# Performance work log

Hardware: AMD Instinct MI355X
Metric: run time of the kernel (lower is better)

The kernel has to match this reference:

```python
import jax, jax.numpy as jnp
import numpy as np

N = 50000
NFEAT = 512
HID = 128
E = 1_600_000


def spmm(row, col, val, dense):
    # sparse [N,N] (COO) @ dense [N,D] -> [N,D]
    gathered = val[:, None] * dense[col]           # [E, D]
    return jax.ops.segment_sum(gathered, row, num_segments=N)


def setup_inputs() -> dict:
    key = jax.random.key(0)
    ks = jax.random.split(key, 12)
    x = jax.random.normal(ks[0], (N, NFEAT), dtype=jnp.float32)
    adj_row = jax.random.randint(ks[1], (E,), 0, N, dtype=jnp.int32)
    adj_col = jax.random.randint(ks[2], (E,), 0, N, dtype=jnp.int32)
    adj_val = jax.random.uniform(ks[3], (E,), dtype=jnp.float32)
    adj_inv_row = jax.random.randint(ks[4], (E,), 0, N, dtype=jnp.int32)
    adj_inv_col = jax.random.randint(ks[5], (E,), 0, N, dtype=jnp.int32)
    adj_inv_val = jax.random.uniform(ks[6], (E,), dtype=jnp.float32)
    # Glorot-ish init for GCN weights
    W1 = jax.random.normal(ks[7], (NFEAT, HID), dtype=jnp.float32) * (1.0 / np.sqrt(NFEAT))
    b1 = jnp.zeros((HID,), dtype=jnp.float32)
    W2 = jax.random.normal(ks[8], (HID, NFEAT), dtype=jnp.float32) * (1.0 / np.sqrt(HID))
    b2 = jnp.zeros((NFEAT,), dtype=jnp.float32)
    return dict(x=x, adj_row=adj_row, adj_col=adj_col, adj_val=adj_val,
                adj_inv_row=adj_inv_row, adj_inv_col=adj_inv_col, adj_inv_val=adj_inv_val,
                W1=W1, b1=b1, W2=W2, b2=b2)


def reference(x, adj_row, adj_col, adj_val, adj_inv_row, adj_inv_col, adj_inv_val,
              W1, b1, W2, b2):
    # Encoder GCN layer: relu( adj @ (x @ W1) + b1 )
    h = jax.nn.relu(spmm(adj_row, adj_col, adj_val, x @ W1) + b1)   # [N, 128]
    embedding = h
    # Decoder GCN layer: relu( adj_inv @ (h @ W2) + b2 )
    out = jax.nn.relu(spmm(adj_inv_row, adj_inv_col, adj_inv_val, h @ W2) + b2)  # [N, nfeat]
    return (out, embedding)
```

## Files before the change

### kernel.cpp

```cpp
#include <hip/hip_runtime.h>

#define NN     50000
#define NFEAT  512
#define HIDD   128
#define NE     1600000
#define NB     ((NN + 255) / 256)
#define NPART  8
#define RPP    (NN / NPART)

typedef __attribute__((ext_vector_type(8))) short    bf16x8;
typedef __attribute__((ext_vector_type(4))) float    f32x4;
typedef __attribute__((ext_vector_type(4))) unsigned short us4;

__device__ inline unsigned short f2bf(float f) {
  unsigned int u = __float_as_uint(f);
  u += 0x7FFFu + ((u >> 16) & 1u);
  return (unsigned short)(u >> 16);
}

__device__ inline float bf2f(unsigned short h) {
  return __uint_as_float((unsigned int)h << 16);
}

__device__ inline void fma4(float4& a, float v, const float4& d) {
  a.x = fmaf(v, d.x, a.x);
  a.y = fmaf(v, d.y, a.y);
  a.z = fmaf(v, d.z, a.z);
  a.w = fmaf(v, d.w, a.w);
}

__device__ inline void fma4b(float4& a, float v, us4 d) {
  a.x = fmaf(v, bf2f(d[0]), a.x);
  a.y = fmaf(v, bf2f(d[1]), a.y);
  a.z = fmaf(v, bf2f(d[2]), a.z);
  a.w = fmaf(v, bf2f(d[3]), a.w);
}

__global__ __launch_bounds__(256) void hist_kernel(
    const int* __restrict__ row, int* __restrict__ counts, int e) {
  int i = blockIdx.x * blockDim.x + threadIdx.x;
  if (i < e) atomicAdd(&counts[row[i]], 1);
}

__global__ __launch_bounds__(256) void block_sum_kernel(
    const int* __restrict__ counts, int* __restrict__ bsum, int n) {
  __shared__ int ws[4];
  int i = blockIdx.x * 256 + threadIdx.x;
  int lane = threadIdx.x & 63, wid = threadIdx.x >> 6;
  int v = (i < n) ? counts[i] : 0;
#pragma unroll
  for (int off = 32; off > 0; off >>= 1) v += __shfl_down(v, off, 64);
  if (lane == 0) ws[wid] = v;
  __syncthreads();
  if (threadIdx.x == 0) bsum[blockIdx.x] = ws[0] + ws[1] + ws[2] + ws[3];
}

__global__ __launch_bounds__(256) void scan_partials_kernel(
    int* __restrict__ bsum, int* __restrict__ rowptr, int nb, int nfull) {
  __shared__ int ws[4];
  int t = threadIdx.x;
  int lane = t & 63, wid = t >> 6;
  int v = (t < nb) ? bsum[t] : 0;
  int incl = v;
#pragma unroll
  for (int off = 1; off < 64; off <<= 1) {
    int u = __shfl_up(incl, off, 64);
    if (lane >= off) incl += u;
  }
  if (lane == 63) ws[wid] = incl;
  __syncthreads();
  int wprefix = 0;
  for (int w = 0; w < wid; ++w) wprefix += ws[w];
  incl += wprefix;
  if (t < nb) bsum[t] = incl - v;
  if (t == nb - 1) rowptr[nfull] = incl;
}

__global__ __launch_bounds__(256) void scan_apply_kernel(
    int* __restrict__ counts, const int* __restrict__ bsum,
    int* __restrict__ rowptr, int n) {
  __shared__ int ws[4];
  int i = blockIdx.x * 256 + threadIdx.x;
  int lane = threadIdx.x & 63, wid = threadIdx.x >> 6;
  int v = (i < n) ? counts[i] : 0;
  int incl = v;
#pragma unroll
  for (int off = 1; off < 64; off <<= 1) {
    int u = __shfl_up(incl, off, 64);
    if (lane >= off) incl += u;
  }
  if (lane == 63) ws[wid] = incl;
  __syncthreads();
  int wprefix = 0;
  for (int w = 0; w < wid; ++w) wprefix += ws[w];
  int excl = bsum[blockIdx.x] + wprefix + (incl - v);
  if (i < n) { rowptr[i] = excl; counts[i] = excl; }
}

__global__ __launch_bounds__(256) void scatter_part_kernel(
    const int* __restrict__ row, const int* __restrict__ col,
    const float* __restrict__ val, int* __restrict__ wptr,
    int2* __restrict__ pairs, int e) {
  int part = blockIdx.x & (NPART - 1);
  int q    = blockIdx.x >> 3;
  int Q    = gridDim.x >> 3;
  int lo = part * RPP, hi = lo + RPP;
  for (int i = q * 256 + threadIdx.x; i < e; i += Q * 256) {
    int r = row[i];
    if (r >= lo && r < hi) {
      int p = atomicAdd(&wptr[r], 1);
      pairs[p] = make_int2(col[i], __float_as_int(val[i]));
    }
  }
}

template <bool DB16, bool EPI, bool WF32, bool WB16>
__global__ __launch_bounds__(256) void spmm_kernel(
    const int* __restrict__ rowptr, const int2* __restrict__ pairs,
    const void* __restrict__ dense, const float* __restrict__ bias,
    float* __restrict__ outf, unsigned short* __restrict__ outb, int n) {
  int r = blockIdx.x * 8 + (threadIdx.x >> 5);
  if (r >= n) return;
  int c4 = (threadIdx.x & 31);
  int s = rowptr[r], e = rowptr[r + 1];
  float4 a0 = make_float4(0.f, 0.f, 0.f, 0.f);
  float4 a1 = a0, a2 = a0, a3 = a0;
  int j = s;
  if constexpr (DB16) {
    const unsigned short* d16 = (const unsigned short*)dense;
    for (; j + 8 <= e; j += 8) {
      int2 p0 = pairs[j + 0], p1 = pairs[j + 1], p2 = pairs[j + 2], p3 = pairs[j + 3];
      int2 p4 = pairs[j + 4], p5 = pairs[j + 5], p6 = pairs[j + 6], p7 = pairs[j + 7];
      us4 d0 = *(const us4*)(d16 + (size_t)p0.x * 128 + c4 * 4);
      us4 d1 = *(const us4*)(d16 + (size_t)p1.x * 128 + c4 * 4);
      us4 d2 = *(const us4*)(d16 + (size_t)p2.x * 128 + c4 * 4);
      us4 d3 = *(const us4*)(d16 + (size_t)p3.x * 128 + c4 * 4);
      us4 d4 = *(const us4*)(d16 + (size_t)p4.x * 128 + c4 * 4);
      us4 d5 = *(const us4*)(d16 + (size_t)p5.x * 128 + c4 * 4);
      us4 d6 = *(const us4*)(d16 + (size_t)p6.x * 128 + c4 * 4);
      us4 d7 = *(const us4*)(d16 + (size_t)p7.x * 128 + c4 * 4);
      fma4b(a0, __int_as_float(p0.y), d0);
      fma4b(a1, __int_as_float(p1.y), d1);
      fma4b(a2, __int_as_float(p2.y), d2);
      fma4b(a3, __int_as_float(p3.y), d3);
      fma4b(a0, __int_as_float(p4.y), d4);
      fma4b(a1, __int_as_float(p5.y), d5);
      fma4b(a2, __int_as_float(p6.y), d6);
      fma4b(a3, __int_as_float(p7.y), d7);
    }
    for (; j < e; ++j) {
      int2 ev = pairs[j];
      us4 d = *(const us4*)(d16 + (size_t)ev.x * 128 + c4 * 4);
      fma4b(a0, __int_as_float(ev.y), d);
    }
  } else {
    const float4* dense4 = (const float4*)dense;
    for (; j + 8 <= e; j += 8) {
      int2 p0 = pairs[j + 0], p1 = pairs[j + 1], p2 = pairs[j + 2], p3 = pairs[j + 3];
      int2 p4 = pairs[j + 4], p5 = pairs[j + 5], p6 = pairs[j + 6], p7 = pairs[j + 7];
      float4 d0 = dense4[(size_t)p0.x * 32 + c4];
      float4 d1 = dense4[(size_t)p1.x * 32 + c4];
      float4 d2 = dense4[(size_t)p2.x * 32 + c4];
      float4 d3 = dense4[(size_t)p3.x * 32 + c4];
      float4 d4 = dense4[(size_t)p4.x * 32 + c4];
      float4 d5 = dense4[(size_t)p5.x * 32 + c4];
      float4 d6 = dense4[(size_t)p6.x * 32 + c4];
      float4 d7 = dense4[(size_t)p7.x * 32 + c4];
      fma4(a0, __int_as_float(p0.y), d0);
      fma4(a1, __int_as_float(p1.y), d1);
      fma4(a2, __int_as_float(p2.y), d2);
      fma4(a3, __int_as_float(p3.y), d3);
      fma4(a0, __int_as_float(p4.y), d4);
      fma4(a1, __int_as_float(p5.y), d5);
      fma4(a2, __int_as_float(p6.y), d6);
      fma4(a3, __int_as_float(p7.y), d7);
    }
    for (; j < e; ++j) {
      int2 ev = pairs[j];
      float4 d = dense4[(size_t)ev.x * 32 + c4];
      fma4(a0, __int_as_float(ev.y), d);
    }
  }
  float4 acc;
  acc.x = (a0.x + a1.x) + (a2.x + a3.x);
  acc.y = (a0.y + a1.y) + (a2.y + a3.y);
  acc.z = (a0.z + a1.z) + (a2.z + a3.z);
  acc.w = (a0.w + a1.w) + (a2.w + a3.w);
  if (EPI) {
    float4 b = ((const float4*)bias)[c4];
    acc.x = fmaxf(acc.x + b.x, 0.f);
    acc.y = fmaxf(acc.y + b.y, 0.f);
    acc.z = fmaxf(acc.z + b.z, 0.f);
    acc.w = fmaxf(acc.w + b.w, 0.f);
  }
  if (WF32)
    *(float4*)(outf + (size_t)r * 128 + c4 * 4) = acc;
  if (WB16) {
    us4 h = {f2bf(acc.x), f2bf(acc.y), f2bf(acc.z), f2bf(acc.w)};
    *(us4*)(outb + (size_t)r * 128 + c4 * 4) = h;
  }
}

template <int K, int N, bool EPI, bool ABF16, bool OUTB>
__global__ __launch_bounds__(256) void gemm_mfma_kernel(
    const void* __restrict__ Av, const float* __restrict__ B,
    const float* __restrict__ bias, void* __restrict__ Cv, int M) {
  __shared__ __align__(16) unsigned short Alds[4096];
  __shared__ __align__(16) unsigned short Blds[4096];
  int tid = threadIdx.x;
  int lane = tid & 63, wid = tid >> 6;
  int wm = wid >> 1, wn = wid & 1;
  int rowBase = blockIdx.x * 128;
  int colBase = blockIdx.y * 128;
  int kg = tid & 7, mrow = tid >> 3;
  int aquad = kg >> 1, aj0 = (kg & 1) * 4;
  int bn = tid & 127, kh = tid >> 7;
  int NTb = bn >> 4, nloc = bn & 15;

  f32x4 acc[4][4];
#pragma unroll
  for (int mt = 0; mt < 4; ++mt)
#pragma unroll
    for (int nt = 0; nt < 4; ++nt)
      acc[mt][nt] = (f32x4){0.f, 0.f, 0.f, 0.f};

  for (int kb = 0; kb < K; kb += 32) {
    float4 av[4];
    us4 av16[4];
    if constexpr (ABF16) {
      const unsigned short* A = (const unsigned short*)Av;
#pragma unroll
      for (int p = 0; p < 4; ++p) {
        int r = rowBase + p * 32 + mrow;
        av16[p] = (r < M) ? *(const us4*)(A + (size_t)r * K + kb + kg * 4)
                          : (us4){0, 0, 0, 0};
      }
    } else {
      const float* A = (const float*)Av;
#pragma unroll
      for (int p = 0; p < 4; ++p) {
        int r = rowBase + p * 32 + mrow;
        av[p] = (r < M) ? *(const float4*)(A + (size_t)r * K + kb + kg * 4)
                        : make_float4(0.f, 0.f, 0.f, 0.f);
      }
    }
    float bv[4][4];
#pragma unroll
    for (int p = 0; p < 4; ++p) {
      int k = p * 8 + kh * 4;
#pragma unroll
      for (int i = 0; i < 4; ++i)
        bv[p][i] = B[(size_t)(kb + k + i) * N + colBase + bn];
    }
    __syncthreads();
#pragma unroll
    for (int p = 0; p < 4; ++p) {
      int m = p * 32 + mrow;
      int MT = m >> 4, mloc = m & 15;
      us4 h;
      if constexpr (ABF16) h = av16[p];
      else h = (us4){f2bf(av[p].x), f2bf(av[p].y), f2bf(av[p].z), f2bf(av[p].w)};
      *(us4*)&Alds[(((MT * 4 + aquad) * 16 + mloc) << 3) + aj0] = h;
    }
#pragma unroll
    for (int p = 0; p < 4; ++p) {
      us4 h = {f2bf(bv[p][0]), f2bf(bv[p][1]), f2bf(bv[p][2]), f2bf(bv[p][3])};
      *(us4*)&Blds[(((NTb * 4 + p) * 16 + nloc) << 3) + kh * 4] = h;
    }
    __syncthreads();
    bf16x8 af[4], bf[4];
#pragma unroll
    for (int mt = 0; mt < 4; ++mt)
      af[mt] = *(bf16x8*)&Alds[(((wm * 4 + mt) * 64 + lane)) << 3];
#pragma unroll
    for (int nt = 0; nt < 4; ++nt)
      bf[nt] = *(bf16x8*)&Blds[(((wn * 4 + nt) * 64 + lane)) << 3];
#pragma unroll
    for (int mt = 0; mt < 4; ++mt)
#pragma unroll
      for (int nt = 0; nt < 4; ++nt)
        acc[mt][nt] = __builtin_amdgcn_mfma_f32_16x16x32_bf16(
            af[mt], bf[nt], acc[mt][nt], 0, 0, 0);
  }
  int cquad = lane >> 4, cn = lane & 15;
#pragma unroll
  for (int nt = 0; nt < 4; ++nt) {
    int col = colBase + wn * 64 + nt * 16 + cn;
    float bb = EPI ? bias[col] : 0.f;
#pragma unroll
    for (int mt = 0; mt < 4; ++mt) {
      int r0 = rowBase + wm * 64 + mt * 16 + cquad * 4;
#pragma unroll
      for (int i = 0; i < 4; ++i) {
        int r = r0 + i;
        if (r < M) {
          float o = acc[mt][nt][i];
          if (EPI) o = fmaxf(o + bb, 0.f);
          if constexpr (OUTB)
            ((unsigned short*)Cv)[(size_t)r * N + col] = f2bf(o);
          else
            ((float*)Cv)[(size_t)r * N + col] = o;
        }
      }
    }
  }
}

extern "C" void kernel_launch(void* const* d_in, const int* in_sizes, int n_in,
                              void* d_out, int out_size, void* d_ws, size_t ws_size,
                              hipStream_t stream) {
  const float* x        = (const float*)d_in[0];
  const int*   adj_row  = (const int*)d_in[1];
  const int*   adj_col  = (const int*)d_in[2];
  const float* adj_val  = (const float*)d_in[3];
  const int*   ainv_row = (const int*)d_in[4];
  const int*   ainv_col = (const int*)d_in[5];
  const float* ainv_val = (const float*)d_in[6];
  const float* W1       = (const float*)d_in[7];
  const float* b1       = (const float*)d_in[8];
  const float* W2       = (const float*)d_in[9];
  const float* b2       = (const float*)d_in[10];

  float* out = (float*)d_out;
  float* emb = out + (size_t)NN * NFEAT;

  size_t off = 0;
  auto carve = [&](size_t bytes) {
    void* p = (char*)d_ws + off;
    off += (bytes + 255) & ~(size_t)255;
    return p;
  };
  unsigned short* Tb   = (unsigned short*)carve((size_t)NN * HIDD * 2);
  unsigned short* H0b  = (unsigned short*)carve((size_t)NN * HIDD * 2);
  int*  rowptr_a = (int*)carve(50004 * 4);
  int*  rowptr_b = (int*)carve(50004 * 4);
  int*  wptr_a   = (int*)carve(50004 * 4);
  int*  wptr_b   = (int*)carve(50004 * 4);
  int*  bsum_a   = (int*)carve(256 * 4);
  int*  bsum_b   = (int*)carve(256 * 4);
  int2* pairs_a  = (int2*)carve((size_t)NE * 8);
  int2* pairs_b  = (int2*)carve((size_t)NE * 8);
  unsigned short* embb = (unsigned short*)((char*)d_ws + off);
  bool full = ws_size >= off + (size_t)NN * HIDD * 2;

  hipMemsetAsync(wptr_a, 0, NN * sizeof(int), stream);
  hipMemsetAsync(wptr_b, 0, NN * sizeof(int), stream);
  hist_kernel<<<NE / 256, 256, 0, stream>>>(adj_row, wptr_a, NE);
  hist_kernel<<<NE / 256, 256, 0, stream>>>(ainv_row, wptr_b, NE);
  block_sum_kernel<<<NB, 256, 0, stream>>>(wptr_a, bsum_a, NN);
  block_sum_kernel<<<NB, 256, 0, stream>>>(wptr_b, bsum_b, NN);
  scan_partials_kernel<<<1, 256, 0, stream>>>(bsum_a, rowptr_a, NB, NN);
  scan_partials_kernel<<<1, 256, 0, stream>>>(bsum_b, rowptr_b, NB, NN);
  scan_apply_kernel<<<NB, 256, 0, stream>>>(wptr_a, bsum_a, rowptr_a, NN);
  scan_apply_kernel<<<NB, 256, 0, stream>>>(wptr_b, bsum_b, rowptr_b, NN);
  scatter_part_kernel<<<2048, 256, 0, stream>>>(adj_row, adj_col, adj_val,
                                                wptr_a, pairs_a, NE);
  scatter_part_kernel<<<2048, 256, 0, stream>>>(ainv_row, ainv_col, ainv_val,
                                                wptr_b, pairs_b, NE);

  gemm_mfma_kernel<NFEAT, HIDD, false, false, true>
      <<<dim3((NN + 127) / 128, 1), 256, 0, stream>>>(x, W1, nullptr, H0b, NN);

  if (full)
    spmm_kernel<true, true, true, true><<<(NN + 7) / 8, 256, 0, stream>>>(
        rowptr_a, pairs_a, H0b, b1, emb, embb, NN);
  else
    spmm_kernel<true, true, true, false><<<(NN + 7) / 8, 256, 0, stream>>>(
        rowptr_a, pairs_a, H0b, b1, emb, nullptr, NN);

  if (full)
    spmm_kernel<true, false, false, true><<<(NN + 7) / 8, 256, 0, stream>>>(
        rowptr_b, pairs_b, embb, nullptr, nullptr, Tb, NN);
  else
    spmm_kernel<false, false, false, true><<<(NN + 7) / 8, 256, 0, stream>>>(
        rowptr_b, pairs_b, emb, nullptr, nullptr, Tb, NN);

  gemm_mfma_kernel<HIDD, NFEAT, true, true, false>
      <<<dim3((NN + 127) / 128, 4), 256, 0, stream>>>(Tb, W2, b2, out, NN);
}
```

Baseline: 711.3 us.

## Record per-edge rank in histogram pass and merge paired CSR-build launches

The histogram kernel now stores each edge's atomicAdd return value as its rank within its row. The scatter pass then places each edge at rowptr[row]+rank without a second round of atomics and without the eight-way row-partitioned multi-pass scan. The two adjacency builds are also merged into single launches using blockIdx.y, which halves the number of launches for each CSR-build stage. In exchange it adds two rank arrays of NE ints (extra workspace and memory traffic), and each pair is written with a 64-bit atomicExch instead of a plain store.

Measured after the change: 684.6 us. 3.8% less time.

```diff
diff --git a/kernel.cpp b/kernel.cpp
--- a/kernel.cpp
+++ b/kernel.cpp
@@ -5,8 +5,6 @@
 #define HIDD   128
 #define NE     1600000
 #define NB     ((NN + 255) / 256)
-#define NPART  8
-#define RPP    (NN / NPART)
 
 typedef __attribute__((ext_vector_type(8))) short    bf16x8;
 typedef __attribute__((ext_vector_type(4))) float    f32x4;
@@ -36,14 +34,22 @@
   a.w = fmaf(v, bf2f(d[3]), a.w);
 }
 
-__global__ __launch_bounds__(256) void hist_kernel(
-    const int* __restrict__ row, int* __restrict__ counts, int e) {
-  int i = blockIdx.x * blockDim.x + threadIdx.x;
-  if (i < e) atomicAdd(&counts[row[i]], 1);
+__global__ __launch_bounds__(256) void hist_rank_kernel(
+    const int* __restrict__ rowA, const int* __restrict__ rowB,
+    int* __restrict__ cntA, int* __restrict__ cntB,
+    int* __restrict__ rnkA, int* __restrict__ rnkB, int e) {
+  const int* row = blockIdx.y ? rowB : rowA;
+  int*       cnt = blockIdx.y ? cntB : cntA;
+  int*       rnk = blockIdx.y ? rnkB : rnkA;
+  int i = blockIdx.x * 256 + threadIdx.x;
+  if (i < e) rnk[i] = atomicAdd(&cnt[row[i]], 1);
 }
 
 __global__ __launch_bounds__(256) void block_sum_kernel(
-    const int* __restrict__ counts, int* __restrict__ bsum, int n) {
+    const int* __restrict__ cntA, const int* __restrict__ cntB,
+    int* __restrict__ bsumA, int* __restrict__ bsumB, int n) {
+  const int* counts = blockIdx.y ? cntB : cntA;
+  int*       bsum   = blockIdx.y ? bsumB : bsumA;
   __shared__ int ws[4];
   int i = blockIdx.x * 256 + threadIdx.x;
   int lane = threadIdx.x & 63, wid = threadIdx.x >> 6;
@@ -56,7 +62,10 @@
 }
 
 __global__ __launch_bounds__(256) void scan_partials_kernel(
-    int* __restrict__ bsum, int* __restrict__ rowptr, int nb, int nfull) {
+    int* __restrict__ bsumA, int* __restrict__ bsumB,
+    int* __restrict__ rpA, int* __restrict__ rpB, int nb, int nfull) {
+  int* bsum   = blockIdx.x ? bsumB : bsumA;
+  int* rowptr = blockIdx.x ? rpB : rpA;
   __shared__ int ws[4];
   int t = threadIdx.x;
   int lane = t & 63, wid = t >> 6;
@@ -77,8 +86,12 @@
 }
 
 __global__ __launch_bounds__(256) void scan_apply_kernel(
-    int* __restrict__ counts, const int* __restrict__ bsum,
-    int* __restrict__ rowptr, int n) {
+    const int* __restrict__ cntA, const int* __restrict__ cntB,
+    const int* __restrict__ bsumA, const int* __restrict__ bsumB,
+    int* __restrict__ rpA, int* __restrict__ rpB, int n) {
+  const int* counts = blockIdx.y ? cntB : cntA;
+  const int* bsum   = blockIdx.y ? bsumB : bsumA;
+  int*       rowptr = blockIdx.y ? rpB : rpA;
   __shared__ int ws[4];
   int i = blockIdx.x * 256 + threadIdx.x;
   int lane = threadIdx.x & 63, wid = threadIdx.x >> 6;
@@ -93,24 +106,29 @@
   __syncthreads();
   int wprefix = 0;
   for (int w = 0; w < wid; ++w) wprefix += ws[w];
-  int excl = bsum[blockIdx.x] + wprefix + (incl - v);
-  if (i < n) { rowptr[i] = excl; counts[i] = excl; }
-}
-
-__global__ __launch_bounds__(256) void scatter_part_kernel(
-    const int* __restrict__ row, const int* __restrict__ col,
-    const float* __restrict__ val, int* __restrict__ wptr,
-    int2* __restrict__ pairs, int e) {
-  int part = blockIdx.x & (NPART - 1);
-  int q    = blockIdx.x >> 3;
-  int Q    = gridDim.x >> 3;
-  int lo = part * RPP, hi = lo + RPP;
-  for (int i = q * 256 + threadIdx.x; i < e; i += Q * 256) {
-    int r = row[i];
-    if (r >= lo && r < hi) {
-      int p = atomicAdd(&wptr[r], 1);
-      pairs[p] = make_int2(col[i], __float_as_int(val[i]));
-    }
+  if (i < n) rowptr[i] = bsum[blockIdx.x] + wprefix + (incl - v);
+}
+
+__global__ __launch_bounds__(256) void scatter_rank_kernel(
+    const int* __restrict__ rowA, const int* __restrict__ colA,
+    const float* __restrict__ valA, const int* __restrict__ rnkA,
+    const int* __restrict__ rpA, int2* __restrict__ pairsA,
+    const int* __restrict__ rowB, const int* __restrict__ colB,
+    const float* __restrict__ valB, const int* __restrict__ rnkB,
+    const int* __restrict__ rpB, int2* __restrict__ pairsB, int e) {
+  const int*   row   = blockIdx.y ? rowB : rowA;
+  const int*   col   = blockIdx.y ? colB : colA;
+  const float* val   = blockIdx.y ? valB : valA;
+  const int*   rnk   = blockIdx.y ? rnkB : rnkA;
+  const int*   rp    = blockIdx.y ? rpB : rpA;
+  int2*        pairs = blockIdx.y ? pairsB : pairsA;
+  int i = blockIdx.x * 256 + threadIdx.x;
+  if (i < e) {
+    int p = rp[row[i]] + rnk[i];
+    unsigned long long v =
+        (unsigned long long)(unsigned int)col[i] |
+        ((unsigned long long)(unsigned int)__float_as_uint(val[i]) << 32);
+    atomicExch((unsigned long long*)&pairs[p], v);
   }
 }
 
@@ -334,29 +352,29 @@
   unsigned short* H0b  = (unsigned short*)carve((size_t)NN * HIDD * 2);
   int*  rowptr_a = (int*)carve(50004 * 4);
   int*  rowptr_b = (int*)carve(50004 * 4);
-  int*  wptr_a   = (int*)carve(50004 * 4);
-  int*  wptr_b   = (int*)carve(50004 * 4);
+  int*  cnt_a    = (int*)carve(50004 * 4);
+  int*  cnt_b    = (int*)carve(50004 * 4);
   int*  bsum_a   = (int*)carve(256 * 4);
   int*  bsum_b   = (int*)carve(256 * 4);
+  int*  rank_a   = (int*)carve((size_t)NE * 4);
+  int*  rank_b   = (int*)carve((size_t)NE * 4);
   int2* pairs_a  = (int2*)carve((size_t)NE * 8);
   int2* pairs_b  = (int2*)carve((size_t)NE * 8);
   unsigned short* embb = (unsigned short*)((char*)d_ws + off);
   bool full = ws_size >= off + (size_t)NN * HIDD * 2;
 
-  hipMemsetAsync(wptr_a, 0, NN * sizeof(int), stream);
-  hipMemsetAsync(wptr_b, 0, NN * sizeof(int), stream);
-  hist_kernel<<<NE / 256, 256, 0, stream>>>(adj_row, wptr_a, NE);
-  hist_kernel<<<NE / 256, 256, 0, stream>>>(ainv_row, wptr_b, NE);
-  block_sum_kernel<<<NB, 256, 0, stream>>>(wptr_a, bsum_a, NN);
-  block_sum_kernel<<<NB, 256, 0, stream>>>(wptr_b, bsum_b, NN);
-  scan_partials_kernel<<<1, 256, 0, stream>>>(bsum_a, rowptr_a, NB, NN);
-  scan_partials_kernel<<<1, 256, 0, stream>>>(bsum_b, rowptr_b, NB, NN);
-  scan_apply_kernel<<<NB, 256, 0, stream>>>(wptr_a, bsum_a, rowptr_a, NN);
-  scan_apply_kernel<<<NB, 256, 0, stream>>>(wptr_b, bsum_b, rowptr_b, NN);
-  scatter_part_kernel<<<2048, 256, 0, stream>>>(adj_row, adj_col, adj_val,
-                                                wptr_a, pairs_a, NE);
-  scatter_part_kernel<<<2048, 256, 0, stream>>>(ainv_row, ainv_col, ainv_val,
-                                                wptr_b, pairs_b, NE);
+  hipMemsetAsync(cnt_a, 0, NN * sizeof(int), stream);
+  hipMemsetAsync(cnt_b, 0, NN * sizeof(int), stream);
+  hist_rank_kernel<<<dim3(NE / 256, 2), 256, 0, stream>>>(
+      adj_row, ainv_row, cnt_a, cnt_b, rank_a, rank_b, NE);
+  block_sum_kernel<<<dim3(NB, 2), 256, 0, stream>>>(cnt_a, cnt_b, bsum_a, bsum_b, NN);
+  scan_partials_kernel<<<2, 256, 0, stream>>>(bsum_a, bsum_b, rowptr_a, rowptr_b,
+                                              NB, NN);
+  scan_apply_kernel<<<dim3(NB, 2), 256, 0, stream>>>(
+      cnt_a, cnt_b, bsum_a, bsum_b, rowptr_a, rowptr_b, NN);
+  scatter_rank_kernel<<<dim3(NE / 256, 2), 256, 0, stream>>>(
+      adj_row, adj_col, adj_val, rank_a, rowptr_a, pairs_a,
+      ainv_row, ainv_col, ainv_val, rank_b, rowptr_b, pairs_b, NE);
 
   gemm_mfma_kernel<NFEAT, HIDD, false, false, true>
       <<<dim3((NN + 127) / 128, 1), 256, 0, stream>>>(x, W1, nullptr, H0b, NN);
```
